# Kernel optimization log

Hardware: AMD Instinct MI355X
Metric: run time of the kernel (lower is better)

## Reference

```python
import jax, jax.numpy as jnp
from jax import lax
import numpy as np

S = 0.025
EPS = 1e-6


def setup_inputs() -> dict:
    key = jax.random.key(0)
    k1, = jax.random.split(key, 1)
    B, F, T = 64, 128, 4000
    x = jax.random.uniform(k1, (B, F, T), dtype=jnp.float32)  # nonnegative spectrogram
    log_gain = jnp.zeros((F,), dtype=jnp.float32)
    log_bias = jnp.zeros((F,), dtype=jnp.float32)
    log_power = jnp.zeros((F,), dtype=jnp.float32)
    return {"x": x, "log_gain": log_gain, "log_bias": log_bias, "log_power": log_power}


def _ema(x):
    # x: [B, F, T]; first-order IIR m_t = (1-s)*m_{t-1} + s*x_t, m_{-1} = x_0
    # (so m_0 = x_0, matching the torch loop's init last_state = x[:, :, 0]).
    xt = jnp.moveaxis(x, -1, 0)  # [T, B, F]

    def step(carry, x_t):
        m = (1.0 - S) * carry + S * x_t
        return m, m

    _, m = lax.scan(step, xt[0], xt)
    return jnp.moveaxis(m, 0, -1)  # [B, F, T]


def reference(x, log_gain, log_bias, log_power):
    m = _ema(x)
    g = jnp.exp(log_gain)[None, :, None]   # [1, F, 1]
    b = jnp.exp(log_bias)[None, :, None]
    p = jnp.exp(log_power)[None, :, None]
    return (x / (m + EPS) ** g + b) ** p - b ** p
```

## Files before the change

kernel.cpp:

```cpp
#include <hip/hip_runtime.h>


#define LOG2F(v) __builtin_amdgcn_logf(v)
#define EXP2F(v) __builtin_amdgcn_exp2f(v)

constexpr int   T_LEN = 4000;
constexpr int   F_DIM = 128;
constexpr int   EPT   = 16;
constexpr int   TPB   = 256;
constexpr int   ACTIVE = T_LEN / EPT;
constexpr float S_C   = 0.025f;
constexpr float A1    = 1.0f - S_C;
constexpr float EPS_C = 1e-6f;

constexpr float pow_n(double a, int n) {
    double r = 1.0;
    for (int i = 0; i < n; ++i) r *= a;
    return (float)r;
}
constexpr float A16 = pow_n((double)A1, EPT);

__global__ __launch_bounds__(TPB) void pcen_kernel(
    const float* __restrict__ x,
    const float* __restrict__ log_gain,
    const float* __restrict__ log_bias,
    const float* __restrict__ log_power,
    float* __restrict__ out)
{
    const int row  = blockIdx.x;
    const int f    = row & (F_DIM - 1);
    const long long base = (long long)row * T_LEN;
    const int tid  = threadIdx.x;
    const int lane = tid & 63;
    const int wid  = tid >> 6;
    const bool active = tid < ACTIVE;

    const float g  = expf(log_gain[f]);
    const float b  = expf(log_bias[f]);
    const float p  = expf(log_power[f]);
    const float bp = EXP2F(p * LOG2F(b));

    float xv[EPT];
    const float4* xin = reinterpret_cast<const float4*>(x + base) + tid * 4;
    if (active) {
        #pragma unroll
        for (int q = 0; q < 4; ++q) {
            float4 v = xin[q];
            xv[q*4 + 0] = v.x; xv[q*4 + 1] = v.y;
            xv[q*4 + 2] = v.z; xv[q*4 + 3] = v.w;
        }
    }

    float Bi = 0.0f;
    if (active) {
        #pragma unroll
        for (int j = 0; j < EPT; ++j) Bi = fmaf(A1, Bi, S_C * xv[j]);
    }
    float Ai = active ? A16 : 1.0f;

    #pragma unroll
    for (int d = 1; d < 64; d <<= 1) {
        float Ap = __shfl_up(Ai, d);
        float Bp = __shfl_up(Bi, d);
        if (lane >= d) { Bi = fmaf(Ai, Bp, Bi); Ai *= Ap; }
    }

    __shared__ float sA[4], sB[4], sM0;
    if (lane == 63) { sA[wid] = Ai; sB[wid] = Bi; }
    if (tid == 0)   { sM0 = xv[0]; }
    __syncthreads();

    float pA = 1.0f, pB = 0.0f;
    for (int w = 0; w < wid; ++w) { pB = fmaf(sA[w], pB, sB[w]); pA *= sA[w]; }

    float eA = __shfl_up(Ai, 1);
    float eB = __shfl_up(Bi, 1);
    if (lane == 0) { eA = 1.0f; eB = 0.0f; }

    float m = fmaf(eA, fmaf(pA, sM0, pB), eB);

    if (active) {
        float4* o4 = reinterpret_cast<float4*>(out + base) + tid * 4;
        #pragma unroll
        for (int q = 0; q < 4; ++q) {
            float4 o;
            float ov[4];
            #pragma unroll
            for (int j = 0; j < 4; ++j) {
                const float xj = xv[q*4 + j];
                m = fmaf(A1, m, S_C * xj);
                float v = xj * EXP2F(-g * LOG2F(m + EPS_C));
                ov[j] = EXP2F(p * LOG2F(v + b)) - bp;
            }
            o.x = ov[0]; o.y = ov[1]; o.z = ov[2]; o.w = ov[3];
            o4[q] = o;
        }
    }
}

extern "C" void kernel_launch(void* const* d_in, const int* in_sizes, int n_in,
                              void* d_out, int out_size, void* d_ws, size_t ws_size,
                              hipStream_t stream) {
    const float* x  = (const float*)d_in[0];
    const float* lg = (const float*)d_in[1];
    const float* lb = (const float*)d_in[2];
    const float* lp = (const float*)d_in[3];
    float* out = (float*)d_out;

    const int rows = in_sizes[0] / T_LEN;
    pcen_kernel<<<dim3(rows), dim3(TPB), 0, stream>>>(x, lg, lb, lp, out);
}
```

Baseline: 238.4 us.

## Use 1024-thread blocks with 4 elements per thread and a two-level wave scan

Each row is now handled by 1024 threads that each process one float4, instead of 256 threads each processing 16 elements. The inter-wave combine becomes a shuffle scan over 16 wave totals followed by an extra barrier, replacing the serial loop. Each thread does a shorter serial chain and loads are fully coalesced, which should expose more parallelism and memory-level concurrency. The cost is larger blocks with fewer resident per CU, an additional __syncthreads, and more scan depth relative to useful work.

```diff
diff --git a/kernel.cpp b/kernel.cpp
--- a/kernel.cpp
+++ b/kernel.cpp
@@ -4,21 +4,14 @@
 #define LOG2F(v) __builtin_amdgcn_logf(v)
 #define EXP2F(v) __builtin_amdgcn_exp2f(v)
 
-constexpr int   T_LEN = 4000;
-constexpr int   F_DIM = 128;
-constexpr int   EPT   = 16;
-constexpr int   TPB   = 256;
-constexpr int   ACTIVE = T_LEN / EPT;
-constexpr float S_C   = 0.025f;
-constexpr float A1    = 1.0f - S_C;
-constexpr float EPS_C = 1e-6f;
-
-constexpr float pow_n(double a, int n) {
-    double r = 1.0;
-    for (int i = 0; i < n; ++i) r *= a;
-    return (float)r;
-}
-constexpr float A16 = pow_n((double)A1, EPT);
+constexpr int   T_LEN  = 4000;
+constexpr int   F_DIM  = 128;
+constexpr int   TPB    = 1024;
+constexpr int   ACTIVE = T_LEN / 4;
+constexpr float S_C    = 0.025f;
+constexpr float A1     = 1.0f - S_C;
+constexpr float EPS_C  = 1e-6f;
+constexpr float A4     = A1 * A1 * A1 * A1;
 
 __global__ __launch_bounds__(TPB) void pcen_kernel(
     const float* __restrict__ x,
@@ -33,30 +26,24 @@
     const int tid  = threadIdx.x;
     const int lane = tid & 63;
     const int wid  = tid >> 6;
-    const bool active = tid < ACTIVE;
+    const bool act = tid < ACTIVE;
 
     const float g  = expf(log_gain[f]);
     const float b  = expf(log_bias[f]);
     const float p  = expf(log_power[f]);
     const float bp = EXP2F(p * LOG2F(b));
 
-    float xv[EPT];
-    const float4* xin = reinterpret_cast<const float4*>(x + base) + tid * 4;
-    if (active) {
-        #pragma unroll
-        for (int q = 0; q < 4; ++q) {
-            float4 v = xin[q];
-            xv[q*4 + 0] = v.x; xv[q*4 + 1] = v.y;
-            xv[q*4 + 2] = v.z; xv[q*4 + 3] = v.w;
-        }
-    }
+    float4 xv = make_float4(0.f, 0.f, 0.f, 0.f);
+    if (act) xv = reinterpret_cast<const float4*>(x + base)[tid];
 
     float Bi = 0.0f;
-    if (active) {
-        #pragma unroll
-        for (int j = 0; j < EPT; ++j) Bi = fmaf(A1, Bi, S_C * xv[j]);
+    if (act) {
+        Bi = S_C * xv.x;
+        Bi = fmaf(A1, Bi, S_C * xv.y);
+        Bi = fmaf(A1, Bi, S_C * xv.z);
+        Bi = fmaf(A1, Bi, S_C * xv.w);
     }
-    float Ai = active ? A16 : 1.0f;
+    float Ai = act ? A4 : 1.0f;
 
     #pragma unroll
     for (int d = 1; d < 64; d <<= 1) {
@@ -65,36 +52,46 @@
         if (lane >= d) { Bi = fmaf(Ai, Bp, Bi); Ai *= Ap; }
     }
 
-    __shared__ float sA[4], sB[4], sM0;
+    __shared__ float sA[16], sB[16], sPA[16], sPB[16], sM0;
     if (lane == 63) { sA[wid] = Ai; sB[wid] = Bi; }
-    if (tid == 0)   { sM0 = xv[0]; }
+    if (tid == 0)   { sM0 = xv.x; }
     __syncthreads();
 
-    float pA = 1.0f, pB = 0.0f;
-    for (int w = 0; w < wid; ++w) { pB = fmaf(sA[w], pB, sB[w]); pA *= sA[w]; }
+    if (wid == 0 && lane < 16) {
+        float a  = sA[lane];
+        float bb = sB[lane];
+        #pragma unroll
+        for (int d = 1; d < 16; d <<= 1) {
+            float ap = __shfl_up(a, d);
+            float bpp = __shfl_up(bb, d);
+            if (lane >= d) { bb = fmaf(a, bpp, bb); a *= ap; }
+        }
+        float ea = __shfl_up(a, 1);
+        float eb = __shfl_up(bb, 1);
+        if (lane == 0) { ea = 1.0f; eb = 0.0f; }
+        sPA[lane] = ea;
+        sPB[lane] = eb;
+    }
+    __syncthreads();
 
+    const float pA = sPA[wid];
+    const float pB = sPB[wid];
     float eA = __shfl_up(Ai, 1);
     float eB = __shfl_up(Bi, 1);
     if (lane == 0) { eA = 1.0f; eB = 0.0f; }
-
     float m = fmaf(eA, fmaf(pA, sM0, pB), eB);
 
-    if (active) {
-        float4* o4 = reinterpret_cast<float4*>(out + base) + tid * 4;
+    if (act) {
+        float xs[4] = { xv.x, xv.y, xv.z, xv.w };
+        float ov[4];
         #pragma unroll
-        for (int q = 0; q < 4; ++q) {
-            float4 o;
-            float ov[4];
-            #pragma unroll
-            for (int j = 0; j < 4; ++j) {
-                const float xj = xv[q*4 + j];
-                m = fmaf(A1, m, S_C * xj);
-                float v = xj * EXP2F(-g * LOG2F(m + EPS_C));
-                ov[j] = EXP2F(p * LOG2F(v + b)) - bp;
-            }
-            o.x = ov[0]; o.y = ov[1]; o.z = ov[2]; o.w = ov[3];
-            o4[q] = o;
+        for (int j = 0; j < 4; ++j) {
+            m = fmaf(A1, m, S_C * xs[j]);
+            float v = xs[j] * EXP2F(-g * LOG2F(m + EPS_C));
+            ov[j]   = EXP2F(p * LOG2F(v + b)) - bp;
         }
+        float4 o = make_float4(ov[0], ov[1], ov[2], ov[3]);
+        reinterpret_cast<float4*>(out + base)[tid] = o;
     }
 }
 
```

Measured after the change: 227.8 us. 1.05x faster.
